# Kernel optimization log

Hardware: AMD Instinct MI355X
Metric: run time of the kernel (lower is better)

## Reference

```python
import jax, jax.numpy as jnp
import numpy as np

WD, WH, WW = 1, 8, 8           # window size
NH = 2                          # num heads
EPS = 1e-5                      # torch LayerNorm default


def _layernorm(x, g, b):
    mu = jnp.mean(x, axis=-1, keepdims=True)
    var = jnp.mean((x - mu) ** 2, axis=-1, keepdims=True)
    return (x - mu) * jax.lax.rsqrt(var + EPS) * g + b


def setup_inputs() -> dict:
    key = jax.random.key(0)
    ks = jax.random.split(key, 12)
    C, H = 192, 768  # dim, mlp hidden
    w = lambda k, shape: (jax.random.normal(k, shape, jnp.float32) * 0.02)
    return {
        "x": jax.random.normal(ks[0], (2, 8, 96, 96, C), jnp.float32),
        "norm3_g": jnp.ones((C,), jnp.float32),
        "norm3_b": jnp.zeros((C,), jnp.float32),
        "in_proj_w": w(ks[1], (3 * C, C)),
        "in_proj_b": jnp.zeros((3 * C,), jnp.float32),
        "out_proj_w": w(ks[2], (C, C)),
        "out_proj_b": jnp.zeros((C,), jnp.float32),
        "norm4_g": jnp.ones((C,), jnp.float32),
        "norm4_b": jnp.zeros((C,), jnp.float32),
        "fc1_w": w(ks[3], (H, C)),
        "fc1_b": jnp.zeros((H,), jnp.float32),
        "fc2_w": w(ks[4], (C, H)),
        "fc2_b": jnp.zeros((C,), jnp.float32),
    }


def _part3(x, norm3_g, norm3_b, in_proj_w, in_proj_b, out_proj_w, out_proj_b):
    B, D, H, W, C = x.shape
    Dn, Hn, Wn = D // WD, H // WH, W // WW
    P = Hn * Wn          # spatial windows
    Wt = WD * WH * WW    # tokens per window (64)
    L = Dn * Wt          # attention sequence length

    xn = _layernorm(x, norm3_g, norm3_b)
    # window partition: (B, Dn, Hn, Wn, wd, wh, ww, C)
    xw = xn.reshape(B, Dn, WD, Hn, WH, Wn, WW, C).transpose(0, 1, 3, 5, 2, 4, 6, 7)
    # tgt: (B, Dn, P, Wt, C) -> h: (B*P, Dn*Wt, C)
    tgt = xw.reshape(B, Dn, P, Wt, C)
    h = tgt.transpose(0, 2, 1, 3, 4).reshape(B * P, L, C)

    # qkv projection (torch Linear convention: x @ W.T + b)
    qkv = h @ in_proj_w.T + in_proj_b          # (Bp, L, 3C)
    q, k, v = jnp.split(qkv, 3, axis=-1)
    hd = C // NH
    q = q.reshape(B * P, L, NH, hd)
    k = k.reshape(B * P, L, NH, hd)
    v = v.reshape(B * P, L, NH, hd)

    # block-causal mask over temporal index (each block is Wt x Wt)
    neg_inf = jnp.finfo(jnp.float32).min
    tmask = jnp.triu(jnp.full((Dn, Dn), neg_inf, jnp.float32), k=1)
    mask = jnp.repeat(jnp.repeat(tmask, Wt, axis=0), Wt, axis=1)  # (L, L)

    scale = 1.0 / np.sqrt(hd)
    scores = jnp.einsum("blhd,bmhd->bhlm", q * scale, k) + mask
    attn = jax.nn.softmax(scores, axis=-1)
    out = jnp.einsum("bhlm,bmhd->blhd", attn, v).reshape(B * P, L, C)
    out = out @ out_proj_w.T + out_proj_b

    # reverse: (B, P, Dn, Wt, C) -> windows -> (B, D, H, W, C)
    out = out.reshape(B, P, Dn, Wt, C).transpose(0, 2, 1, 3, 4)
    out = out.reshape(B, Dn, Hn, Wn, WD, WH, WW, C)
    out = out.transpose(0, 1, 4, 2, 5, 3, 6, 7).reshape(B, D, H, W, C)
    return out


def reference(x, norm3_g, norm3_b, in_proj_w, in_proj_b, out_proj_w, out_proj_b,
              norm4_g, norm4_b, fc1_w, fc1_b, fc2_w, fc2_b):
    x = x + _part3(x, norm3_g, norm3_b, in_proj_w, in_proj_b, out_proj_w, out_proj_b)
    xn = _layernorm(x, norm4_g, norm4_b)
    mlp = jax.nn.gelu(xn @ fc1_w.T + fc1_b, approximate=False) @ fc2_w.T + fc2_b
    return x + mlp
```

## Files before the change

### kernel.cpp

```cpp
#include <hip/hip_runtime.h>
#include <cstdint>
#include <cstddef>


typedef float   f32x4  __attribute__((ext_vector_type(4)));
typedef __bf16  bf16x8 __attribute__((ext_vector_type(8)));
typedef unsigned int   u32x4  __attribute__((ext_vector_type(4)));
typedef unsigned short u16x4  __attribute__((ext_vector_type(4)));

#define DEVI __device__ __forceinline__

DEVI float bf2f(unsigned short u) {
    union { unsigned int i; float f; } v; v.i = ((unsigned int)u) << 16; return v.f;
}
DEVI unsigned short f2bf(float f) {
    unsigned int u = __builtin_bit_cast(unsigned int, f);
    unsigned int r = u + 0x7fffu + ((u >> 16) & 1u);
    return (unsigned short)(r >> 16);
}
DEVI float gelu_fast(float v) {
    float t = v * v;
    float z = v * (1.5957691216057308f + 0.07135481627f * t);
    float e = __expf(z);
    float r = 2.0f / (1.0f + e);
    return v - 0.5f * v * r;
}

typedef __attribute__((address_space(3))) unsigned char       lds_u8;
typedef __attribute__((address_space(1))) const unsigned char g_u8;
DEVI void gl_lds16(const void* g, void* l) {
    __builtin_amdgcn_global_load_lds((g_u8*)g, (lds_u8*)l, 16, 0, 0);
}

__global__ __launch_bounds__(256) void k_wconv(const float* __restrict__ wqkv,
                                               const float* __restrict__ wout,
                                               const float* __restrict__ wfc1,
                                               const float* __restrict__ wfc2,
                                               unsigned short* __restrict__ oq,
                                               unsigned short* __restrict__ oo,
                                               unsigned short* __restrict__ o1,
                                               unsigned short* __restrict__ o2) {
    int i = blockIdx.x * 256 + threadIdx.x;
    if (i < 122880) {
        int r = i / 192;
        oq[i] = (r < 576) ? f2bf(wqkv[i]) : (unsigned short)0;
    } else if (i < 172032) {
        int j = i - 122880; int r = j / 192;
        oo[j] = (r < 192) ? f2bf(wout[j]) : (unsigned short)0;
    } else if (i < 319488) {
        int j = i - 172032;
        o1[j] = f2bf(wfc1[j]);
    } else if (i < 516096) {
        int j = i - 319488; int r = j / 768;
        o2[j] = (r < 192) ? f2bf(wfc2[j]) : (unsigned short)0;
    }
}

__global__ __launch_bounds__(256) void k_ln3(const float* __restrict__ x,
                                             const float* __restrict__ g,
                                             const float* __restrict__ bsh,
                                             unsigned short* __restrict__ h) {
    int w = threadIdx.x >> 6, lane = threadIdx.x & 63;
    int token = blockIdx.x * 4 + w;
    const float* xp = x + (size_t)token * 192;
    float v0 = xp[lane], v1 = xp[lane + 64], v2 = xp[lane + 128];
    float s = v0 + v1 + v2;
#pragma unroll
    for (int off = 32; off; off >>= 1) s += __shfl_xor(s, off);
    float mean = s * (1.f / 192.f);
    float d0 = v0 - mean, d1 = v1 - mean, d2 = v2 - mean;
    float q = d0 * d0 + d1 * d1 + d2 * d2;
#pragma unroll
    for (int off = 32; off; off >>= 1) q += __shfl_xor(q, off);
    float rs = rsqrtf(q * (1.f / 192.f) + 1e-5f);
    int b  = token / (8 * 96 * 96);
    int r0 = token - b * (8 * 96 * 96);
    int d  = r0 / (96 * 96);
    int r1 = r0 - d * (96 * 96);
    int hh = r1 / 96;
    int ww = r1 - hh * 96;
    int bp = b * 144 + (hh >> 3) * 12 + (ww >> 3);
    int l  = d * 64 + (hh & 7) * 8 + (ww & 7);
    unsigned short* hp = h + ((size_t)bp * 512 + l) * 192;
    hp[lane]       = f2bf(d0 * rs * g[lane]       + bsh[lane]);
    hp[lane + 64]  = f2bf(d1 * rs * g[lane + 64]  + bsh[lane + 64]);
    hp[lane + 128] = f2bf(d2 * rs * g[lane + 128] + bsh[lane + 128]);
}

__global__ __launch_bounds__(256) void k_ln4b(const unsigned short* __restrict__ yb,
                                              const float* __restrict__ g,
                                              const float* __restrict__ bsh,
                                              unsigned short* __restrict__ xn) {
    int sub = threadIdx.x >> 5, tl = threadIdx.x & 31;
    size_t row = (size_t)blockIdx.x * 8 + sub;
    const unsigned int* rp = reinterpret_cast<const unsigned int*>(yb + row * 192);
    float v[6];
#pragma unroll
    for (int j = 0; j < 3; j++) {
        unsigned int w = rp[tl + 32 * j];
        v[2 * j]     = bf2f((unsigned short)(w & 0xffffu));
        v[2 * j + 1] = bf2f((unsigned short)(w >> 16));
    }
    float s = v[0] + v[1] + v[2] + v[3] + v[4] + v[5];
#pragma unroll
    for (int off = 1; off < 32; off <<= 1) s += __shfl_xor(s, off);
    float mean = s * (1.f / 192.f);
    float q = 0.f;
#pragma unroll
    for (int j = 0; j < 6; j++) { v[j] -= mean; q += v[j] * v[j]; }
#pragma unroll
    for (int off = 1; off < 32; off <<= 1) q += __shfl_xor(q, off);
    float rs = rsqrtf(q * (1.f / 192.f) + 1e-5f);
    unsigned int* op = reinterpret_cast<unsigned int*>(xn + row * 192);
#pragma unroll
    for (int j = 0; j < 3; j++) {
        int c = (tl + 32 * j) * 2;
        unsigned short lo = f2bf(v[2 * j]     * rs * g[c]     + bsh[c]);
        unsigned short hi = f2bf(v[2 * j + 1] * rs * g[c + 1] + bsh[c + 1]);
        op[tl + 32 * j] = ((unsigned int)hi << 16) | lo;
    }
}

template <int EPI, int K, int NF>
__global__ __launch_bounds__(256) void k_gemm128(const unsigned short* __restrict__ A,
                                                 const unsigned short* __restrict__ Bw,
                                                 const float* __restrict__ bias,
                                                 unsigned short* __restrict__ outb,
                                                 unsigned short* __restrict__ vt,
                                                 float* __restrict__ outf,
                                                 const float* __restrict__ res,
                                                 const unsigned short* __restrict__ resb) {
    constexpr int BN = NF * 32;
    __shared__ unsigned short As[2][128 * 64];
    __shared__ unsigned short Bs[2][BN * 64];
    const int tid = threadIdx.x;
    const int nwg = gridDim.x * gridDim.y;
    const int flat = blockIdx.y * gridDim.x + blockIdx.x;
    const int swz = (flat & 7) * (nwg >> 3) + (flat >> 3);
    const int bx = swz % gridDim.x, by = swz / gridDim.x;
    const int row0 = by * 128, col0 = bx * BN;
    const int wv = tid >> 6, lane = tid & 63, lr = lane & 15, lg = lane >> 4;
    const int wr = wv >> 1, wc = wv & 1;
    const int sr = lane >> 3, sc = lane & 7;
    f32x4 acc[4][NF] = {};

    auto stage = [&](int t, int buf) {
        int k0 = t * 64;
#pragma unroll
        for (int i = 0; i < 4; i++) {
            int gq = wv * 4 + i;
            int r = gq * 8 + sr;
            int j = sc ^ (r & 7);
            gl_lds16(A + (size_t)(row0 + r) * K + k0 + j * 8, &As[buf][gq * 512]);
        }
#pragma unroll
        for (int i = 0; i < NF; i++) {
            int gq = wv * NF + i;
            int r = gq * 8 + sr;
            int j = sc ^ (r & 7);
            gl_lds16(Bw + (size_t)(col0 + r) * K + k0 + j * 8, &Bs[buf][gq * 512]);
        }
    };

    const int NT = K / 64;
    stage(0, 0);
    for (int t = 0; t < NT; ++t) {
        int cur = t & 1;
        if (t + 1 < NT) {
            stage(t + 1, cur ^ 1);
            if constexpr (NF == 4) asm volatile("s_waitcnt vmcnt(8)" ::: "memory");
            else                   asm volatile("s_waitcnt vmcnt(10)" ::: "memory");
        } else {
            asm volatile("s_waitcnt vmcnt(0)" ::: "memory");
        }
        __builtin_amdgcn_sched_barrier(0);
        __builtin_amdgcn_s_barrier();
        __builtin_amdgcn_sched_barrier(0);
#pragma unroll
        for (int kk = 0; kk < 64; kk += 32) {
            bf16x8 af[4], bf[NF];
#pragma unroll
            for (int m = 0; m < 4; m++) {
                int r = wr * 64 + m * 16 + lr;
                int j = ((kk >> 3) + lg) ^ (r & 7);
                af[m] = __builtin_bit_cast(bf16x8,
                    *reinterpret_cast<const u32x4*>(&As[cur][r * 64 + j * 8]));
            }
#pragma unroll
            for (int n = 0; n < NF; n++) {
                int r = wc * (NF * 16) + n * 16 + lr;
                int j = ((kk >> 3) + lg) ^ (r & 7);
                bf[n] = __builtin_bit_cast(bf16x8,
                    *reinterpret_cast<const u32x4*>(&Bs[cur][r * 64 + j * 8]));
            }
#pragma unroll
            for (int m = 0; m < 4; m++)
#pragma unroll
                for (int n = 0; n < NF; n++)
                    acc[m][n] = __builtin_amdgcn_mfma_f32_16x16x32_bf16(bf[n], af[m], acc[m][n], 0, 0, 0);
        }
        __builtin_amdgcn_sched_barrier(0);
        __builtin_amdgcn_s_barrier();
        __builtin_amdgcn_sched_barrier(0);
    }

#pragma unroll
    for (int m = 0; m < 4; m++) {
        const int arow = row0 + wr * 64 + m * 16 + lr;
#pragma unroll
        for (int n = 0; n < NF; n++) {
            const int colb = col0 + wc * (NF * 16) + n * 16 + lg * 4;
            if constexpr (EPI == 0) {
                if (colb < 384) {
                    f32x4 b4 = *reinterpret_cast<const f32x4*>(bias + colb);
                    float sc2 = (colb < 192) ? 0.1020620726159658f : 1.f;
                    u16x4 pk;
#pragma unroll
                    for (int rr = 0; rr < 4; rr++) pk[rr] = f2bf((acc[m][n][rr] + b4[rr]) * sc2);
                    *reinterpret_cast<u16x4*>(outb + (size_t)arow * 384 + colb) = pk;
                } else if (colb < 576) {
                    int head = (colb >= 480) ? 1 : 0;
                    int bp = arow >> 9, tok = arow & 511;
                    size_t vb = ((size_t)(bp * 2 + head) * 96 + (colb - 384 - head * 96)) * 512 + tok;
#pragma unroll
                    for (int rr = 0; rr < 4; rr++)
                        vt[vb + (size_t)rr * 512] = f2bf(acc[m][n][rr] + bias[colb + rr]);
                }
            } else if constexpr (EPI == 1) {
                if (colb < 192) {
                    int bp = arow >> 9, l = arow & 511;
                    int bb = bp / 144, p = bp - bb * 144;
                    int hn = p / 12, wn = p - hn * 12;
                    int dn = l >> 6, t_ = l & 63;
                    size_t tok = ((size_t)((bb * 8 + dn) * 96 + hn * 8 + (t_ >> 3)) * 96 + wn * 8 + (t_ & 7));
                    size_t idx = tok * 192 + colb;
                    f32x4 r4 = *reinterpret_cast<const f32x4*>(res + idx);
                    f32x4 b4 = *reinterpret_cast<const f32x4*>(bias + colb);
                    u16x4 pk;
#pragma unroll
                    for (int rr = 0; rr < 4; rr++) pk[rr] = f2bf(r4[rr] + acc[m][n][rr] + b4[rr]);
                    *reinterpret_cast<u16x4*>(outb + idx) = pk;
                }
            } else if constexpr (EPI == 2) {
                f32x4 b4 = *reinterpret_cast<const f32x4*>(bias + colb);
                u16x4 pk;
#pragma unroll
                for (int rr = 0; rr < 4; rr++) pk[rr] = f2bf(gelu_fast(acc[m][n][rr] + b4[rr]));
                *reinterpret_cast<u16x4*>(outb + (size_t)arow * 768 + colb) = pk;
            } else {
                f32x4 b4 = *reinterpret_cast<const f32x4*>(bias + colb);
                u16x4 rb = *reinterpret_cast<const u16x4*>(resb + (size_t)arow * 192 + colb);
                f32x4 o4;
#pragma unroll
                for (int rr = 0; rr < 4; rr++) o4[rr] = bf2f(rb[rr]) + acc[m][n][rr] + b4[rr];
                *reinterpret_cast<f32x4*>(outf + (size_t)arow * 192 + colb) = o4;
            }
        }
    }
}

__global__ __launch_bounds__(512) void k_attn(const unsigned short* __restrict__ qk,
                                              const unsigned short* __restrict__ vt,
                                              unsigned short* __restrict__ aout) {
    __shared__ unsigned short Ks[64][104];
    __shared__ unsigned short Vs[96][72];
    __shared__ unsigned short Ps[8][16][72];

    int bid = (blockIdx.x & 7) * 288 + (blockIdx.x >> 3);
    int bp = bid >> 3, rest = bid & 7, head = rest >> 2, pr = rest & 3;
    int tid = threadIdx.x, wv = tid >> 6, lane = tid & 63;
    int lr = lane & 15, lg = lane >> 4;
    int wq = wv & 3, wt = wv >> 2;
    int nk = 2 * pr + 2;

    size_t qrow0 = (size_t)bp * 512 + (size_t)(2 * pr + wt) * 64;
    const unsigned short* vbase = vt + (size_t)(bp * 2 + head) * 96 * 512;
    size_t krowb = (size_t)bp * 512;

    bf16x8 qf[3];
    {
        const unsigned short* qp = qk + (qrow0 + wq * 16 + lr) * 384 + head * 96 + lg * 8;
#pragma unroll
        for (int ks = 0; ks < 3; ks++)
            qf[ks] = __builtin_bit_cast(bf16x8, *reinterpret_cast<const u32x4*>(qp + ks * 32));
    }

    f32x4 o[6] = {};
    float m_ = -1e30f, lsum = 0.f;

    u32x4 sreg[3];
    auto issue = [&](int dnk) {
#pragma unroll
        for (int i = 0; i < 3; i++) {
            int c = tid + i * 512;
            if (c < 768) {
                int r = c / 12, cc = c - r * 12;
                sreg[i] = *reinterpret_cast<const u32x4*>(
                    qk + (krowb + dnk * 64 + r) * 384 + 192 + head * 96 + cc * 8);
            } else {
                int c2 = c - 768; int d = c2 >> 3, tb = c2 & 7;
                sreg[i] = *reinterpret_cast<const u32x4*>(
                    vbase + (size_t)d * 512 + dnk * 64 + tb * 8);
            }
        }
    };
    auto commit = [&]() {
#pragma unroll
        for (int i = 0; i < 3; i++) {
            int c = tid + i * 512;
            if (c < 768) {
                int r = c / 12, cc = c - r * 12;
                *reinterpret_cast<u32x4*>(&Ks[r][cc * 8]) = sreg[i];
            } else {
                int c2 = c - 768; int d = c2 >> 3, tb = c2 & 7;
                *reinterpret_cast<u32x4*>(&Vs[d][tb * 8]) = sreg[i];
            }
        }
    };

    issue(0);
    for (int dnk = 0; dnk < nk; ++dnk) {
        commit();
        __syncthreads();
        if (dnk + 1 < nk) issue(dnk + 1);
        if (wt == 1 || dnk < nk - 1) {
            f32x4 st[4] = {};
#pragma unroll
            for (int ks = 0; ks < 3; ks++) {
#pragma unroll
                for (int ct = 0; ct < 4; ct++) {
                    bf16x8 kf = __builtin_bit_cast(bf16x8,
                        *reinterpret_cast<const u32x4*>(&Ks[ct * 16 + lr][ks * 32 + lg * 8]));
                    st[ct] = __builtin_amdgcn_mfma_f32_16x16x32_bf16(kf, qf[ks], st[ct], 0, 0, 0);
                }
            }
            float mx = st[0][0];
#pragma unroll
            for (int ct = 0; ct < 4; ct++)
#pragma unroll
                for (int rr = 0; rr < 4; rr++) mx = fmaxf(mx, st[ct][rr]);
            mx = fmaxf(mx, __shfl_xor(mx, 16));
            mx = fmaxf(mx, __shfl_xor(mx, 32));
            float mnew = fmaxf(m_, mx);
            float corr = __expf(m_ - mnew);
            m_ = mnew;
            float ps = 0.f;
#pragma unroll
            for (int ct = 0; ct < 4; ct++) {
                u16x4 pk;
#pragma unroll
                for (int rr = 0; rr < 4; rr++) {
                    float pv = __expf(st[ct][rr] - mnew);
                    ps += pv;
                    pk[rr] = f2bf(pv);
                }
                *reinterpret_cast<u16x4*>(&Ps[wv][lr][ct * 16 + lg * 4]) = pk;
            }
            ps += __shfl_xor(ps, 16);
            ps += __shfl_xor(ps, 32);
            lsum = lsum * corr + ps;
#pragma unroll
            for (int rr = 0; rr < 4; rr++) {
                float cr = __shfl(corr, (lane & 48) | (lg * 4 + rr));
#pragma unroll
                for (int nf = 0; nf < 6; nf++) o[nf][rr] *= cr;
            }
#pragma unroll
            for (int kk = 0; kk < 2; kk++) {
                bf16x8 pf = __builtin_bit_cast(bf16x8,
                    *reinterpret_cast<const u32x4*>(&Ps[wv][lr][kk * 32 + lg * 8]));
#pragma unroll
                for (int nf = 0; nf < 6; nf++) {
                    bf16x8 vf = __builtin_bit_cast(bf16x8,
                        *reinterpret_cast<const u32x4*>(&Vs[nf * 16 + lr][kk * 32 + lg * 8]));
                    o[nf] = __builtin_amdgcn_mfma_f32_16x16x32_bf16(pf, vf, o[nf], 0, 0, 0);
                }
            }
        }
        __syncthreads();
    }

#pragma unroll
    for (int rr = 0; rr < 4; rr++) {
        float li = __shfl(lsum, (lane & 48) | (lg * 4 + rr));
        float inv = 1.f / li;
        size_t row = qrow0 + wq * 16 + lg * 4 + rr;
#pragma unroll
        for (int nf = 0; nf < 6; nf++)
            aout[row * 192 + head * 96 + nf * 16 + lr] = f2bf(o[nf][rr] * inv);
    }
}

extern "C" void kernel_launch(void* const* d_in, const int* in_sizes, int n_in,
                              void* d_out, int out_size, void* d_ws, size_t ws_size,
                              hipStream_t stream) {
    const float* x    = (const float*)d_in[0];
    const float* n3g  = (const float*)d_in[1];
    const float* n3b  = (const float*)d_in[2];
    const float* wqkv = (const float*)d_in[3];
    const float* bqkv = (const float*)d_in[4];
    const float* wout = (const float*)d_in[5];
    const float* bout = (const float*)d_in[6];
    const float* n4g  = (const float*)d_in[7];
    const float* n4b  = (const float*)d_in[8];
    const float* wfc1 = (const float*)d_in[9];
    const float* bfc1 = (const float*)d_in[10];
    const float* wfc2 = (const float*)d_in[11];
    const float* bfc2 = (const float*)d_in[12];
    float* out = (float*)d_out;

    char* ws = (char*)d_ws;
    unsigned short* qk     = (unsigned short*)(ws + 0);
    unsigned short* vt     = (unsigned short*)(ws + 113246208);
    unsigned short* h      = (unsigned short*)(ws + 169869312);
    unsigned short* attn   = (unsigned short*)(ws + 226492416);
    unsigned short* xn4    = (unsigned short*)(ws + 226492416);
    unsigned short* hidden = (unsigned short*)(ws + 0);
    unsigned short* wq_bf  = (unsigned short*)(ws + 283115520);
    unsigned short* wo_bf  = (unsigned short*)(ws + 283361280);
    unsigned short* w1_bf  = (unsigned short*)(ws + 283459584);
    unsigned short* w2_bf  = (unsigned short*)(ws + 283754496);
    unsigned short* ybf    = (unsigned short*)(ws + 284147712);

    k_wconv<<<2016, 256, 0, stream>>>(wqkv, wout, wfc1, wfc2, wq_bf, wo_bf, w1_bf, w2_bf);
    k_ln3<<<36864, 256, 0, stream>>>(x, n3g, n3b, h);
    k_gemm128<0, 192, 4><<<dim3(5, 1152), 256, 0, stream>>>(h, wq_bf, bqkv, qk, vt, nullptr, nullptr, nullptr);
    k_attn<<<2304, 512, 0, stream>>>(qk, vt, attn);
    k_gemm128<1, 192, 4><<<dim3(2, 1152), 256, 0, stream>>>(attn, wo_bf, bout, ybf, nullptr, nullptr, x, nullptr);
    k_ln4b<<<18432, 256, 0, stream>>>(ybf, n4g, n4b, xn4);
    k_gemm128<2, 192, 4><<<dim3(6, 1152), 256, 0, stream>>>(xn4, w1_bf, bfc1, hidden, nullptr, nullptr, nullptr, nullptr);
    k_gemm128<3, 768, 6><<<dim3(1, 1152), 256, 0, stream>>>(hidden, w2_bf, bfc2, nullptr, nullptr, out, nullptr, ybf);
}
```

Measured before the change: 600.5 us.

## Fold LayerNorm affine into weights and fuse LN into QKV and MLP GEMMs

Folds the LayerNorm gamma into the QKV and fc1 weights and beta into effective biases, so the GEMMs only need the normalized input. LN3 is computed inside the QKV GEMM prologue directly from x with the window gather, which removes the separate h buffer. LN4, fc1, GELU and fc2 are fused into one MLP kernel that keeps the 768-wide hidden tile in LDS, removing the large hidden-activation round trip through HBM. The cost is a long serialized tile loop with two barriers per tile and heavy LDS use, which lowers occupancy. LN variance now uses the single-pass E[x²]−μ² form on bf16-rounded values, which is less precise than the two-pass version.

```diff
diff --git a/kernel.cpp b/kernel.cpp
--- a/kernel.cpp
+++ b/kernel.cpp
@@ -36,140 +36,130 @@
                                                const float* __restrict__ wout,
                                                const float* __restrict__ wfc1,
                                                const float* __restrict__ wfc2,
+                                               const float* __restrict__ n3g,
+                                               const float* __restrict__ n4g,
                                                unsigned short* __restrict__ oq,
                                                unsigned short* __restrict__ oo,
                                                unsigned short* __restrict__ o1,
                                                unsigned short* __restrict__ o2) {
     int i = blockIdx.x * 256 + threadIdx.x;
     if (i < 122880) {
-        int r = i / 192;
-        oq[i] = (r < 576) ? f2bf(wqkv[i]) : (unsigned short)0;
+        int r = i / 192, c = i - r * 192;
+        oq[i] = (r < 576) ? f2bf(wqkv[i] * n3g[c]) : (unsigned short)0;
     } else if (i < 172032) {
         int j = i - 122880; int r = j / 192;
         oo[j] = (r < 192) ? f2bf(wout[j]) : (unsigned short)0;
     } else if (i < 319488) {
-        int j = i - 172032;
-        o1[j] = f2bf(wfc1[j]);
+        int j = i - 172032; int c = j % 192;
+        o1[j] = f2bf(wfc1[j] * n4g[c]);
     } else if (i < 516096) {
         int j = i - 319488; int r = j / 768;
         o2[j] = (r < 192) ? f2bf(wfc2[j]) : (unsigned short)0;
     }
 }
 
-__global__ __launch_bounds__(256) void k_ln3(const float* __restrict__ x,
-                                             const float* __restrict__ g,
-                                             const float* __restrict__ bsh,
-                                             unsigned short* __restrict__ h) {
-    int w = threadIdx.x >> 6, lane = threadIdx.x & 63;
-    int token = blockIdx.x * 4 + w;
-    const float* xp = x + (size_t)token * 192;
-    float v0 = xp[lane], v1 = xp[lane + 64], v2 = xp[lane + 128];
-    float s = v0 + v1 + v2;
+__global__ __launch_bounds__(256) void k_bias(const float* __restrict__ wqkv,
+                                              const float* __restrict__ bqkv,
+                                              const float* __restrict__ n3b,
+                                              const float* __restrict__ wfc1,
+                                              const float* __restrict__ bfc1,
+                                              const float* __restrict__ n4b,
+                                              float* __restrict__ beffq,
+                                              float* __restrict__ beff1) {
+    int wid = blockIdx.x * 4 + (threadIdx.x >> 6);
+    int lane = threadIdx.x & 63;
+    const float* wrow; const float* bb; float base; float* dst;
+    if (wid < 576) { wrow = wqkv + (size_t)wid * 192; bb = n3b; base = bqkv[wid]; dst = beffq + wid; }
+    else { int h = wid - 576; wrow = wfc1 + (size_t)h * 192; bb = n4b; base = bfc1[h]; dst = beff1 + h; }
+    float s = wrow[lane] * bb[lane] + wrow[lane + 64] * bb[lane + 64]
+            + wrow[lane + 128] * bb[lane + 128];
 #pragma unroll
     for (int off = 32; off; off >>= 1) s += __shfl_xor(s, off);
-    float mean = s * (1.f / 192.f);
-    float d0 = v0 - mean, d1 = v1 - mean, d2 = v2 - mean;
-    float q = d0 * d0 + d1 * d1 + d2 * d2;
-#pragma unroll
-    for (int off = 32; off; off >>= 1) q += __shfl_xor(q, off);
-    float rs = rsqrtf(q * (1.f / 192.f) + 1e-5f);
-    int b  = token / (8 * 96 * 96);
-    int r0 = token - b * (8 * 96 * 96);
-    int d  = r0 / (96 * 96);
-    int r1 = r0 - d * (96 * 96);
-    int hh = r1 / 96;
-    int ww = r1 - hh * 96;
-    int bp = b * 144 + (hh >> 3) * 12 + (ww >> 3);
-    int l  = d * 64 + (hh & 7) * 8 + (ww & 7);
-    unsigned short* hp = h + ((size_t)bp * 512 + l) * 192;
-    hp[lane]       = f2bf(d0 * rs * g[lane]       + bsh[lane]);
-    hp[lane + 64]  = f2bf(d1 * rs * g[lane + 64]  + bsh[lane + 64]);
-    hp[lane + 128] = f2bf(d2 * rs * g[lane + 128] + bsh[lane + 128]);
-}
-
-__global__ __launch_bounds__(256) void k_ln4b(const unsigned short* __restrict__ yb,
-                                              const float* __restrict__ g,
-                                              const float* __restrict__ bsh,
-                                              unsigned short* __restrict__ xn) {
-    int sub = threadIdx.x >> 5, tl = threadIdx.x & 31;
-    size_t row = (size_t)blockIdx.x * 8 + sub;
-    const unsigned int* rp = reinterpret_cast<const unsigned int*>(yb + row * 192);
-    float v[6];
-#pragma unroll
-    for (int j = 0; j < 3; j++) {
-        unsigned int w = rp[tl + 32 * j];
-        v[2 * j]     = bf2f((unsigned short)(w & 0xffffu));
-        v[2 * j + 1] = bf2f((unsigned short)(w >> 16));
-    }
-    float s = v[0] + v[1] + v[2] + v[3] + v[4] + v[5];
-#pragma unroll
-    for (int off = 1; off < 32; off <<= 1) s += __shfl_xor(s, off);
-    float mean = s * (1.f / 192.f);
-    float q = 0.f;
-#pragma unroll
-    for (int j = 0; j < 6; j++) { v[j] -= mean; q += v[j] * v[j]; }
-#pragma unroll
-    for (int off = 1; off < 32; off <<= 1) q += __shfl_xor(q, off);
-    float rs = rsqrtf(q * (1.f / 192.f) + 1e-5f);
-    unsigned int* op = reinterpret_cast<unsigned int*>(xn + row * 192);
-#pragma unroll
-    for (int j = 0; j < 3; j++) {
-        int c = (tl + 32 * j) * 2;
-        unsigned short lo = f2bf(v[2 * j]     * rs * g[c]     + bsh[c]);
-        unsigned short hi = f2bf(v[2 * j + 1] * rs * g[c + 1] + bsh[c + 1]);
-        op[tl + 32 * j] = ((unsigned int)hi << 16) | lo;
-    }
-}
-
-template <int EPI, int K, int NF>
-__global__ __launch_bounds__(256) void k_gemm128(const unsigned short* __restrict__ A,
-                                                 const unsigned short* __restrict__ Bw,
-                                                 const float* __restrict__ bias,
-                                                 unsigned short* __restrict__ outb,
-                                                 unsigned short* __restrict__ vt,
-                                                 float* __restrict__ outf,
-                                                 const float* __restrict__ res,
-                                                 const unsigned short* __restrict__ resb) {
-    constexpr int BN = NF * 32;
-    __shared__ unsigned short As[2][128 * 64];
-    __shared__ unsigned short Bs[2][BN * 64];
+    if (lane == 0) *dst = base + s;
+}
+
+__global__ __launch_bounds__(256) void k_qkv(const float* __restrict__ x,
+                                             const unsigned short* __restrict__ Bw,
+                                             const float* __restrict__ beff,
+                                             unsigned short* __restrict__ qk,
+                                             unsigned short* __restrict__ vt) {
+    __shared__ unsigned short As[3][128][64];
+    __shared__ unsigned short Bs[2][128 * 64];
     const int tid = threadIdx.x;
     const int nwg = gridDim.x * gridDim.y;
     const int flat = blockIdx.y * gridDim.x + blockIdx.x;
     const int swz = (flat & 7) * (nwg >> 3) + (flat >> 3);
     const int bx = swz % gridDim.x, by = swz / gridDim.x;
-    const int row0 = by * 128, col0 = bx * BN;
+    const int row0 = by * 128, col0 = bx * 128;
     const int wv = tid >> 6, lane = tid & 63, lr = lane & 15, lg = lane >> 4;
     const int wr = wv >> 1, wc = wv & 1;
     const int sr = lane >> 3, sc = lane & 7;
-    f32x4 acc[4][NF] = {};
-
-    auto stage = [&](int t, int buf) {
+
+    auto stageB = [&](int t, int buf) {
         int k0 = t * 64;
 #pragma unroll
         for (int i = 0; i < 4; i++) {
             int gq = wv * 4 + i;
             int r = gq * 8 + sr;
             int j = sc ^ (r & 7);
-            gl_lds16(A + (size_t)(row0 + r) * K + k0 + j * 8, &As[buf][gq * 512]);
-        }
-#pragma unroll
-        for (int i = 0; i < NF; i++) {
-            int gq = wv * NF + i;
-            int r = gq * 8 + sr;
-            int j = sc ^ (r & 7);
-            gl_lds16(Bw + (size_t)(col0 + r) * K + k0 + j * 8, &Bs[buf][gq * 512]);
+            gl_lds16(Bw + (size_t)(col0 + r) * 192 + k0 + j * 8, &Bs[buf][gq * 512]);
         }
     };
 
-    const int NT = K / 64;
-    stage(0, 0);
-    for (int t = 0; t < NT; ++t) {
-        int cur = t & 1;
-        if (t + 1 < NT) {
-            stage(t + 1, cur ^ 1);
-            if constexpr (NF == 4) asm volatile("s_waitcnt vmcnt(8)" ::: "memory");
-            else                   asm volatile("s_waitcnt vmcnt(10)" ::: "memory");
+    stageB(0, 0);
+    {
+        int ar = tid >> 1, ah = tid & 1;
+        int n = row0 + ar;
+        int bp = n >> 9, l = n & 511;
+        int bb = bp / 144, p = bp - bb * 144;
+        int hn = p / 12, wn = p - hn * 12;
+        int dn = l >> 6, t_ = l & 63;
+        size_t tok = ((size_t)((bb * 8 + dn) * 96 + hn * 8 + (t_ >> 3)) * 96 + wn * 8 + (t_ & 7));
+        const float* src = x + tok * 192;
+        float sum = 0.f, ssq = 0.f;
+#pragma unroll
+        for (int ci = 0; ci < 12; ci++) {
+            int c = ah * 12 + ci;
+            f32x4 a = *reinterpret_cast<const f32x4*>(src + c * 8);
+            f32x4 b = *reinterpret_cast<const f32x4*>(src + c * 8 + 4);
+            u16x4 pa, pb;
+#pragma unroll
+            for (int e = 0; e < 4; e++) {
+                sum += a[e] + b[e]; ssq += a[e] * a[e] + b[e] * b[e];
+                pa[e] = f2bf(a[e]); pb[e] = f2bf(b[e]);
+            }
+            int j = (c & 7) ^ (ar & 7);
+            unsigned short* dst = &As[c >> 3][ar][j * 8];
+            *reinterpret_cast<u16x4*>(dst) = pa;
+            *reinterpret_cast<u16x4*>(dst + 4) = pb;
+        }
+        sum += __shfl_xor(sum, 1); ssq += __shfl_xor(ssq, 1);
+        float mu = sum * (1.f / 192.f);
+        float rs = rsqrtf(ssq * (1.f / 192.f) - mu * mu + 1e-5f);
+#pragma unroll
+        for (int ci = 0; ci < 12; ci++) {
+            int c = ah * 12 + ci;
+            int j = (c & 7) ^ (ar & 7);
+            unsigned short* p8 = &As[c >> 3][ar][j * 8];
+            u16x4 v0 = *reinterpret_cast<u16x4*>(p8);
+            u16x4 v1 = *reinterpret_cast<u16x4*>(p8 + 4);
+#pragma unroll
+            for (int e = 0; e < 4; e++) {
+                v0[e] = f2bf((bf2f(v0[e]) - mu) * rs);
+                v1[e] = f2bf((bf2f(v1[e]) - mu) * rs);
+            }
+            *reinterpret_cast<u16x4*>(p8) = v0;
+            *reinterpret_cast<u16x4*>(p8 + 4) = v1;
+        }
+    }
+    asm volatile("s_waitcnt lgkmcnt(0)" ::: "memory");
+
+    f32x4 acc[4][4] = {};
+#pragma unroll
+    for (int t = 0; t < 3; ++t) {
+        if (t + 1 < 3) {
+            stageB(t + 1, (t + 1) & 1);
+            asm volatile("s_waitcnt vmcnt(4)" ::: "memory");
         } else {
             asm volatile("s_waitcnt vmcnt(0)" ::: "memory");
         }
@@ -178,25 +168,25 @@
         __builtin_amdgcn_sched_barrier(0);
 #pragma unroll
         for (int kk = 0; kk < 64; kk += 32) {
-            bf16x8 af[4], bf[NF];
+            bf16x8 af[4], bf[4];
 #pragma unroll
             for (int m = 0; m < 4; m++) {
                 int r = wr * 64 + m * 16 + lr;
                 int j = ((kk >> 3) + lg) ^ (r & 7);
                 af[m] = __builtin_bit_cast(bf16x8,
-                    *reinterpret_cast<const u32x4*>(&As[cur][r * 64 + j * 8]));
-            }
-#pragma unroll
-            for (int n = 0; n < NF; n++) {
-                int r = wc * (NF * 16) + n * 16 + lr;
+                    *reinterpret_cast<const u32x4*>(&As[t][r][j * 8]));
+            }
+#pragma unroll
+            for (int n = 0; n < 4; n++) {
+                int r = wc * 64 + n * 16 + lr;
                 int j = ((kk >> 3) + lg) ^ (r & 7);
                 bf[n] = __builtin_bit_cast(bf16x8,
-                    *reinterpret_cast<const u32x4*>(&Bs[cur][r * 64 + j * 8]));
+                    *reinterpret_cast<const u32x4*>(&Bs[t & 1][r * 64 + j * 8]));
             }
 #pragma unroll
             for (int m = 0; m < 4; m++)
 #pragma unroll
-                for (int n = 0; n < NF; n++)
+                for (int n = 0; n < 4; n++)
                     acc[m][n] = __builtin_amdgcn_mfma_f32_16x16x32_bf16(bf[n], af[m], acc[m][n], 0, 0, 0);
         }
         __builtin_amdgcn_sched_barrier(0);
@@ -208,52 +198,122 @@
     for (int m = 0; m < 4; m++) {
         const int arow = row0 + wr * 64 + m * 16 + lr;
 #pragma unroll
-        for (int n = 0; n < NF; n++) {
-            const int colb = col0 + wc * (NF * 16) + n * 16 + lg * 4;
-            if constexpr (EPI == 0) {
-                if (colb < 384) {
-                    f32x4 b4 = *reinterpret_cast<const f32x4*>(bias + colb);
-                    float sc2 = (colb < 192) ? 0.1020620726159658f : 1.f;
-                    u16x4 pk;
-#pragma unroll
-                    for (int rr = 0; rr < 4; rr++) pk[rr] = f2bf((acc[m][n][rr] + b4[rr]) * sc2);
-                    *reinterpret_cast<u16x4*>(outb + (size_t)arow * 384 + colb) = pk;
-                } else if (colb < 576) {
-                    int head = (colb >= 480) ? 1 : 0;
-                    int bp = arow >> 9, tok = arow & 511;
-                    size_t vb = ((size_t)(bp * 2 + head) * 96 + (colb - 384 - head * 96)) * 512 + tok;
-#pragma unroll
-                    for (int rr = 0; rr < 4; rr++)
-                        vt[vb + (size_t)rr * 512] = f2bf(acc[m][n][rr] + bias[colb + rr]);
-                }
-            } else if constexpr (EPI == 1) {
-                if (colb < 192) {
-                    int bp = arow >> 9, l = arow & 511;
-                    int bb = bp / 144, p = bp - bb * 144;
-                    int hn = p / 12, wn = p - hn * 12;
-                    int dn = l >> 6, t_ = l & 63;
-                    size_t tok = ((size_t)((bb * 8 + dn) * 96 + hn * 8 + (t_ >> 3)) * 96 + wn * 8 + (t_ & 7));
-                    size_t idx = tok * 192 + colb;
-                    f32x4 r4 = *reinterpret_cast<const f32x4*>(res + idx);
-                    f32x4 b4 = *reinterpret_cast<const f32x4*>(bias + colb);
-                    u16x4 pk;
-#pragma unroll
-                    for (int rr = 0; rr < 4; rr++) pk[rr] = f2bf(r4[rr] + acc[m][n][rr] + b4[rr]);
-                    *reinterpret_cast<u16x4*>(outb + idx) = pk;
-                }
-            } else if constexpr (EPI == 2) {
+        for (int n = 0; n < 4; n++) {
+            const int colb = col0 + wc * 64 + n * 16 + lg * 4;
+            if (colb < 384) {
+                f32x4 b4 = *reinterpret_cast<const f32x4*>(beff + colb);
+                float sc2 = (colb < 192) ? 0.1020620726159658f : 1.f;
+                u16x4 pk;
+#pragma unroll
+                for (int rr = 0; rr < 4; rr++) pk[rr] = f2bf((acc[m][n][rr] + b4[rr]) * sc2);
+                *reinterpret_cast<u16x4*>(qk + (size_t)arow * 384 + colb) = pk;
+            } else if (colb < 576) {
+                int head = (colb >= 480) ? 1 : 0;
+                int bp = arow >> 9, tok = arow & 511;
+                size_t vb = ((size_t)(bp * 2 + head) * 96 + (colb - 384 - head * 96)) * 512 + tok;
+#pragma unroll
+                for (int rr = 0; rr < 4; rr++)
+                    vt[vb + (size_t)rr * 512] = f2bf(acc[m][n][rr] + beff[colb + rr]);
+            }
+        }
+    }
+}
+
+__global__ __launch_bounds__(256) void k_oproj(const unsigned short* __restrict__ A,
+                                               const unsigned short* __restrict__ Bw,
+                                               const float* __restrict__ bias,
+                                               unsigned short* __restrict__ ybf,
+                                               const float* __restrict__ res) {
+    __shared__ unsigned short As[2][128 * 64];
+    __shared__ unsigned short Bs[2][128 * 64];
+    const int tid = threadIdx.x;
+    const int nwg = gridDim.x * gridDim.y;
+    const int flat = blockIdx.y * gridDim.x + blockIdx.x;
+    const int swz = (flat & 7) * (nwg >> 3) + (flat >> 3);
+    const int bx = swz % gridDim.x, by = swz / gridDim.x;
+    const int row0 = by * 128, col0 = bx * 128;
+    const int wv = tid >> 6, lane = tid & 63, lr = lane & 15, lg = lane >> 4;
+    const int wr = wv >> 1, wc = wv & 1;
+    const int sr = lane >> 3, sc = lane & 7;
+    f32x4 acc[4][4] = {};
+
+    auto stage = [&](int t, int buf) {
+        int k0 = t * 64;
+#pragma unroll
+        for (int i = 0; i < 4; i++) {
+            int gq = wv * 4 + i;
+            int r = gq * 8 + sr;
+            int j = sc ^ (r & 7);
+            gl_lds16(A + (size_t)(row0 + r) * 192 + k0 + j * 8, &As[buf][gq * 512]);
+        }
+#pragma unroll
+        for (int i = 0; i < 4; i++) {
+            int gq = wv * 4 + i;
+            int r = gq * 8 + sr;
+            int j = sc ^ (r & 7);
+            gl_lds16(Bw + (size_t)(col0 + r) * 192 + k0 + j * 8, &Bs[buf][gq * 512]);
+        }
+    };
+
+    stage(0, 0);
+#pragma unroll
+    for (int t = 0; t < 3; ++t) {
+        if (t + 1 < 3) {
+            stage(t + 1, (t + 1) & 1);
+            asm volatile("s_waitcnt vmcnt(8)" ::: "memory");
+        } else {
+            asm volatile("s_waitcnt vmcnt(0)" ::: "memory");
+        }
+        __builtin_amdgcn_sched_barrier(0);
+        __builtin_amdgcn_s_barrier();
+        __builtin_amdgcn_sched_barrier(0);
+#pragma unroll
+        for (int kk = 0; kk < 64; kk += 32) {
+            bf16x8 af[4], bf[4];
+#pragma unroll
+            for (int m = 0; m < 4; m++) {
+                int r = wr * 64 + m * 16 + lr;
+                int j = ((kk >> 3) + lg) ^ (r & 7);
+                af[m] = __builtin_bit_cast(bf16x8,
+                    *reinterpret_cast<const u32x4*>(&As[t & 1][r * 64 + j * 8]));
+            }
+#pragma unroll
+            for (int n = 0; n < 4; n++) {
+                int r = wc * 64 + n * 16 + lr;
+                int j = ((kk >> 3) + lg) ^ (r & 7);
+                bf[n] = __builtin_bit_cast(bf16x8,
+                    *reinterpret_cast<const u32x4*>(&Bs[t & 1][r * 64 + j * 8]));
+            }
+#pragma unroll
+            for (int m = 0; m < 4; m++)
+#pragma unroll
+                for (int n = 0; n < 4; n++)
+                    acc[m][n] = __builtin_amdgcn_mfma_f32_16x16x32_bf16(bf[n], af[m], acc[m][n], 0, 0, 0);
+        }
+        __builtin_amdgcn_sched_barrier(0);
+        __builtin_amdgcn_s_barrier();
+        __builtin_amdgcn_sched_barrier(0);
+    }
+
+#pragma unroll
+    for (int m = 0; m < 4; m++) {
+        const int arow = row0 + wr * 64 + m * 16 + lr;
+        int bp = arow >> 9, l = arow & 511;
+        int bb = bp / 144, p = bp - bb * 144;
+        int hn = p / 12, wn = p - hn * 12;
+        int dn = l >> 6, t_ = l & 63;
+        size_t tok = ((size_t)((bb * 8 + dn) * 96 + hn * 8 + (t_ >> 3)) * 96 + wn * 8 + (t_ & 7));
+#pragma unroll
+        for (int n = 0; n < 4; n++) {
+            const int colb = col0 + wc * 64 + n * 16 + lg * 4;
+            if (colb < 192) {
+                size_t idx = tok * 192 + colb;
+                f32x4 r4 = *reinterpret_cast<const f32x4*>(res + idx);
                 f32x4 b4 = *reinterpret_cast<const f32x4*>(bias + colb);
                 u16x4 pk;
 #pragma unroll
-                for (int rr = 0; rr < 4; rr++) pk[rr] = f2bf(gelu_fast(acc[m][n][rr] + b4[rr]));
-                *reinterpret_cast<u16x4*>(outb + (size_t)arow * 768 + colb) = pk;
-            } else {
-                f32x4 b4 = *reinterpret_cast<const f32x4*>(bias + colb);
-                u16x4 rb = *reinterpret_cast<const u16x4*>(resb + (size_t)arow * 192 + colb);
-                f32x4 o4;
-#pragma unroll
-                for (int rr = 0; rr < 4; rr++) o4[rr] = bf2f(rb[rr]) + acc[m][n][rr] + b4[rr];
-                *reinterpret_cast<f32x4*>(outf + (size_t)arow * 192 + colb) = o4;
+                for (int rr = 0; rr < 4; rr++) pk[rr] = f2bf(r4[rr] + acc[m][n][rr] + b4[rr]);
+                *reinterpret_cast<u16x4*>(ybf + idx) = pk;
             }
         }
     }
@@ -388,6 +448,168 @@
 #pragma unroll
         for (int nf = 0; nf < 6; nf++)
             aout[row * 192 + head * 96 + nf * 16 + lr] = f2bf(o[nf][rr] * inv);
+    }
+}
+
+__global__ __launch_bounds__(512) void k_mlp(const unsigned short* __restrict__ ybf,
+                                             const unsigned short* __restrict__ w1,
+                                             const unsigned short* __restrict__ w2,
+                                             const float* __restrict__ beff1,
+                                             const float* __restrict__ b2,
+                                             float* __restrict__ out) {
+    __shared__ unsigned short XN[3][64][64];
+    __shared__ unsigned short Hs[4][16][776];
+    __shared__ unsigned short Ws[2][128 * 64];
+    const int tid = threadIdx.x;
+    const int bid = (blockIdx.x & 7) * 288 + (blockIdx.x >> 3);
+    const int row0 = bid * 64;
+    const int wv = tid >> 6, lane = tid & 63, lr = lane & 15, lg = lane >> 4;
+    const int wr = wv & 3, wc = wv >> 2;
+
+#pragma unroll
+    for (int i = 0; i < 3; i++) {
+        int g = wv * 3 + i;
+        int sub = g >> 3, rg = g & 7;
+        int r = rg * 8 + (lane >> 3);
+        int c = (lane & 7) ^ (r & 7);
+        gl_lds16(ybf + (size_t)(row0 + r) * 192 + sub * 64 + c * 8, &XN[sub][rg * 8][0]);
+    }
+    auto stageW = [&](int tile, int buf) {
+        const unsigned short* src; int ldk, rbase, kbase;
+        if (tile < 18) { int cb = tile / 3, ks = tile - cb * 3; src = w1; ldk = 192; rbase = cb * 128; kbase = ks * 64; }
+        else { int i2 = tile - 18; int oh = i2 / 12, kt = i2 - oh * 12; src = w2; ldk = 768; rbase = oh * 128; kbase = kt * 64; }
+#pragma unroll
+        for (int i = 0; i < 2; i++) {
+            int g = wv * 2 + i;
+            int r = g * 8 + (lane >> 3);
+            int c = (lane & 7) ^ (r & 7);
+            gl_lds16(src + (size_t)(rbase + r) * ldk + kbase + c * 8, &Ws[buf][g * 512]);
+        }
+    };
+    stageW(0, 0);
+    asm volatile("s_waitcnt vmcnt(2)" ::: "memory");
+    __builtin_amdgcn_sched_barrier(0);
+    __builtin_amdgcn_s_barrier();
+    __builtin_amdgcn_sched_barrier(0);
+
+    {
+        int r = tid >> 3, q = tid & 7;
+        float sum = 0.f, ssq = 0.f;
+        u16x4 vv[3][2];
+#pragma unroll
+        for (int ci = 0; ci < 3; ci++) {
+            int c = q * 3 + ci;
+            int j = (c & 7) ^ (r & 7);
+            unsigned short* p8 = &XN[c >> 3][r][j * 8];
+            vv[ci][0] = *reinterpret_cast<u16x4*>(p8);
+            vv[ci][1] = *reinterpret_cast<u16x4*>(p8 + 4);
+#pragma unroll
+            for (int e = 0; e < 4; e++) {
+                float a = bf2f(vv[ci][0][e]), b = bf2f(vv[ci][1][e]);
+                sum += a + b; ssq += a * a + b * b;
+            }
+        }
+        sum += __shfl_xor(sum, 1); ssq += __shfl_xor(ssq, 1);
+        sum += __shfl_xor(sum, 2); ssq += __shfl_xor(ssq, 2);
+        sum += __shfl_xor(sum, 4); ssq += __shfl_xor(ssq, 4);
+        float mu = sum * (1.f / 192.f);
+        float rs = rsqrtf(ssq * (1.f / 192.f) - mu * mu + 1e-5f);
+#pragma unroll
+        for (int ci = 0; ci < 3; ci++) {
+            int c = q * 3 + ci;
+            int j = (c & 7) ^ (r & 7);
+            unsigned short* p8 = &XN[c >> 3][r][j * 8];
+            u16x4 o0, o1;
+#pragma unroll
+            for (int e = 0; e < 4; e++) {
+                o0[e] = f2bf((bf2f(vv[ci][0][e]) - mu) * rs);
+                o1[e] = f2bf((bf2f(vv[ci][1][e]) - mu) * rs);
+            }
+            *reinterpret_cast<u16x4*>(p8) = o0;
+            *reinterpret_cast<u16x4*>(p8 + 4) = o1;
+        }
+    }
+    asm volatile("s_waitcnt lgkmcnt(0)" ::: "memory");
+
+    const f32x4 zf = {0.f, 0.f, 0.f, 0.f};
+    f32x4 acc[4];
+    acc[0] = zf; acc[1] = zf; acc[2] = zf; acc[3] = zf;
+    for (int tile = 0; tile < 42; ++tile) {
+        int buf = tile & 1;
+        if (tile + 1 < 42) {
+            stageW(tile + 1, buf ^ 1);
+            asm volatile("s_waitcnt vmcnt(2)" ::: "memory");
+        } else {
+            asm volatile("s_waitcnt vmcnt(0)" ::: "memory");
+        }
+        __builtin_amdgcn_sched_barrier(0);
+        __builtin_amdgcn_s_barrier();
+        __builtin_amdgcn_sched_barrier(0);
+
+        if (tile < 18) {
+            int cb = tile / 3, ks = tile - cb * 3;
+            if (ks == 0) { acc[0] = zf; acc[1] = zf; acc[2] = zf; acc[3] = zf; }
+            int rA = wr * 16 + lr;
+#pragma unroll
+            for (int kk = 0; kk < 2; kk++) {
+                bf16x8 af = __builtin_bit_cast(bf16x8, *reinterpret_cast<const u32x4*>(
+                    &XN[ks][rA][((kk * 4 + lg) ^ (rA & 7)) * 8]));
+#pragma unroll
+                for (int n = 0; n < 4; n++) {
+                    int rw = wc * 64 + n * 16 + lr;
+                    int j = (kk * 4 + lg) ^ (rw & 7);
+                    bf16x8 bw = __builtin_bit_cast(bf16x8,
+                        *reinterpret_cast<const u32x4*>(&Ws[buf][rw * 64 + j * 8]));
+                    acc[n] = __builtin_amdgcn_mfma_f32_16x16x32_bf16(bw, af, acc[n], 0, 0, 0);
+                }
+            }
+            if (ks == 2) {
+#pragma unroll
+                for (int n = 0; n < 4; n++) {
+                    int hc = cb * 128 + wc * 64 + n * 16 + lg * 4;
+                    f32x4 b4 = *reinterpret_cast<const f32x4*>(beff1 + hc);
+                    u16x4 pk;
+#pragma unroll
+                    for (int rr = 0; rr < 4; rr++) pk[rr] = f2bf(gelu_fast(acc[n][rr] + b4[rr]));
+                    *reinterpret_cast<u16x4*>(&Hs[wr][lr][hc]) = pk;
+                }
+            }
+        } else {
+            int i2 = tile - 18; int oh = i2 / 12, kt = i2 - oh * 12;
+            if (kt == 0) { acc[0] = zf; acc[1] = zf; acc[2] = zf; acc[3] = zf; }
+#pragma unroll
+            for (int kk = 0; kk < 2; kk++) {
+                bf16x8 af = __builtin_bit_cast(bf16x8, *reinterpret_cast<const u32x4*>(
+                    &Hs[wr][lr][kt * 64 + kk * 32 + lg * 8]));
+#pragma unroll
+                for (int n = 0; n < 4; n++) {
+                    int rw = wc * 64 + n * 16 + lr;
+                    int j = (kk * 4 + lg) ^ (rw & 7);
+                    bf16x8 bw = __builtin_bit_cast(bf16x8,
+                        *reinterpret_cast<const u32x4*>(&Ws[buf][rw * 64 + j * 8]));
+                    acc[n] = __builtin_amdgcn_mfma_f32_16x16x32_bf16(bw, af, acc[n], 0, 0, 0);
+                }
+            }
+            if (kt == 11) {
+                int arow = row0 + wr * 16 + lr;
+#pragma unroll
+                for (int n = 0; n < 4; n++) {
+                    int oc = oh * 128 + wc * 64 + n * 16 + lg * 4;
+                    if (oc < 192) {
+                        f32x4 b4 = *reinterpret_cast<const f32x4*>(b2 + oc);
+                        u16x4 rb = *reinterpret_cast<const u16x4*>(ybf + (size_t)arow * 192 + oc);
+                        f32x4 o4;
+#pragma unroll
+                        for (int rr = 0; rr < 4; rr++) o4[rr] = bf2f(rb[rr]) + acc[n][rr] + b4[rr];
+                        *reinterpret_cast<f32x4*>(out + (size_t)arow * 192 + oc) = o4;
+                    }
+                }
+            }
+        }
+        asm volatile("s_waitcnt lgkmcnt(0)" ::: "memory");
+        __builtin_amdgcn_sched_barrier(0);
+        __builtin_amdgcn_s_barrier();
+        __builtin_amdgcn_sched_barrier(0);
     }
 }
 
@@ -410,24 +632,21 @@
     float* out = (float*)d_out;
 
     char* ws = (char*)d_ws;
-    unsigned short* qk     = (unsigned short*)(ws + 0);
-    unsigned short* vt     = (unsigned short*)(ws + 113246208);
-    unsigned short* h      = (unsigned short*)(ws + 169869312);
-    unsigned short* attn   = (unsigned short*)(ws + 226492416);
-    unsigned short* xn4    = (unsigned short*)(ws + 226492416);
-    unsigned short* hidden = (unsigned short*)(ws + 0);
-    unsigned short* wq_bf  = (unsigned short*)(ws + 283115520);
-    unsigned short* wo_bf  = (unsigned short*)(ws + 283361280);
-    unsigned short* w1_bf  = (unsigned short*)(ws + 283459584);
-    unsigned short* w2_bf  = (unsigned short*)(ws + 283754496);
-    unsigned short* ybf    = (unsigned short*)(ws + 284147712);
-
-    k_wconv<<<2016, 256, 0, stream>>>(wqkv, wout, wfc1, wfc2, wq_bf, wo_bf, w1_bf, w2_bf);
-    k_ln3<<<36864, 256, 0, stream>>>(x, n3g, n3b, h);
-    k_gemm128<0, 192, 4><<<dim3(5, 1152), 256, 0, stream>>>(h, wq_bf, bqkv, qk, vt, nullptr, nullptr, nullptr);
+    unsigned short* qk    = (unsigned short*)(ws + 0);
+    unsigned short* vt    = (unsigned short*)(ws + 113246208);
+    unsigned short* attn  = (unsigned short*)(ws + 169869312);
+    unsigned short* ybf   = (unsigned short*)(ws + 226492416);
+    unsigned short* wq_bf = (unsigned short*)(ws + 283115520);
+    unsigned short* wo_bf = (unsigned short*)(ws + 283361280);
+    unsigned short* w1_bf = (unsigned short*)(ws + 283459584);
+    unsigned short* w2_bf = (unsigned short*)(ws + 283754496);
+    float*          beffq = (float*)(ws + 284147712);
+    float*          beff1 = (float*)(ws + 284150016);
+
+    k_wconv<<<2016, 256, 0, stream>>>(wqkv, wout, wfc1, wfc2, n3g, n4g, wq_bf, wo_bf, w1_bf, w2_bf);
+    k_bias<<<336, 256, 0, stream>>>(wqkv, bqkv, n3b, wfc1, bfc1, n4b, beffq, beff1);
+    k_qkv<<<dim3(5, 1152), 256, 0, stream>>>(x, wq_bf, beffq, qk, vt);
     k_attn<<<2304, 512, 0, stream>>>(qk, vt, attn);
-    k_gemm128<1, 192, 4><<<dim3(2, 1152), 256, 0, stream>>>(attn, wo_bf, bout, ybf, nullptr, nullptr, x, nullptr);
-    k_ln4b<<<18432, 256, 0, stream>>>(ybf, n4g, n4b, xn4);
-    k_gemm128<2, 192, 4><<<dim3(6, 1152), 256, 0, stream>>>(xn4, w1_bf, bfc1, hidden, nullptr, nullptr, nullptr, nullptr);
-    k_gemm128<3, 768, 6><<<dim3(1, 1152), 256, 0, stream>>>(hidden, w2_bf, bfc2, nullptr, nullptr, out, nullptr, ybf);
-}
+    k_oproj<<<dim3(2, 1152), 256, 0, stream>>>(attn, wo_bf, bout, ybf, x);
+    k_mlp<<<2304, 512, 0, stream>>>(ybf, w1_bf, w2_bf, beff1, bfc2, out);
+}
```

New measurement: 747.7 us. 24.5% more time.
